# Kernel optimization log

Hardware: AMD Instinct MI355X
Metric: run time of the kernel (lower is better)

The kernel has to match this reference:

```python
import jax, jax.numpy as jnp
import numpy as np

INV_DELTA = 15.0  # init kwarg inv_delta
EPS = 1e-12       # torch F.normalize eps


def setup_inputs() -> dict:
    key = jax.random.key(0)
    k1, k2 = jax.random.split(key)
    features = jax.random.normal(k1, (32, 256, 30, 30), dtype=jnp.float32)
    # _embedding buffer: randn clamped to >= 0
    embedding = jnp.maximum(jax.random.normal(k2, (2048, 256), dtype=jnp.float32), 0.0)
    # _min_distance_mean buffer, initialized to 0.5
    min_distance_mean = jnp.ones((1,), dtype=jnp.float32) * 0.5
    return {"features": features, "embedding": embedding,
            "min_distance_mean": min_distance_mean}


def reference(features, embedding, min_distance_mean):
    # crop 1-pixel border: [B,C,H,W] -> [B,C,H-2,W-2]
    f = features[:, :, 1:-1, 1:-1]
    # squared euclidean distance to each codeword via GEMM trick:
    # dist[b,k,h,w] = ||f[b,:,h,w]||^2 + ||e[k]||^2 - 2 <f, e[k]>
    f2 = jnp.sum(f * f, axis=1, keepdims=True)                 # [B,1,H',W']
    e2 = jnp.sum(embedding * embedding, axis=1)                # [K]
    xe = jnp.einsum('bchw,kc->bkhw', f, embedding)             # 1x1-conv GEMM
    dist = f2 + e2[None, :, None, None] - 2.0 * xe             # [B,K,H',W']
    # adaptive temperature softmax over codewords
    inv_delta_adaptive = INV_DELTA / min_distance_mean[0]
    codes = jax.nn.softmax(-inv_delta_adaptive * dist, axis=1)  # [B,K,H',W']
    # global average pool + L1 normalize
    bow = jnp.mean(codes, axis=(2, 3))                          # [B,K]
    bow = bow / jnp.maximum(jnp.sum(jnp.abs(bow), axis=1, keepdims=True), EPS)
    return (bow, codes)
```

## Files before the change

kernel.cpp:

```cpp
#include <hip/hip_runtime.h>
#include <hip/hip_bf16.h>
#include <math.h>

typedef __attribute__((ext_vector_type(8))) short bf16x8;
typedef __attribute__((ext_vector_type(16))) float f32x16;

#define B_ 32
#define C_ 256
#define K_ 2048
#define HW_ 784
#define NPIX 25088
#define FEAT_BSTRIDE 230400
#define FEAT_CSTRIDE 900
#define INV_DELTA 15.0f
#define LOG2E 1.4426950408889634f
#define QSCALE 409.6f
#define QDEC (LOG2E / QSCALE)

#define BM 128
#define BN 128
#define LSTR 64
#define NSLAB 16

#define AS1 __attribute__((address_space(1)))
#define AS3 __attribute__((address_space(3)))

__device__ __forceinline__ ushort f2bf(float x) {
    __hip_bfloat16 h = __float2bfloat16(x);
    return *reinterpret_cast<ushort*>(&h);
}
__device__ __forceinline__ float bf2f(ushort u) {
    __hip_bfloat16 h;
    *reinterpret_cast<ushort*>(&h) = u;
    return __bfloat162float(h);
}
__device__ __forceinline__ void gl_lds16(const ushort* g, ushort* l) {
    __builtin_amdgcn_global_load_lds((AS1 const uint*)g, (AS3 uint*)l, 16, 0, 0);
}

__global__ void e2_kernel(const float* __restrict__ emb, float* __restrict__ e2) {
    int t = threadIdx.x;
    int wid = t >> 6, lane = t & 63;
    int k = blockIdx.x * 4 + wid;
    const float* er = emb + (size_t)k * C_;
    float v0 = er[lane], v1 = er[lane + 64], v2 = er[lane + 128], v3 = er[lane + 192];
    float s = v0 * v0 + v1 * v1 + v2 * v2 + v3 * v3;
#pragma unroll
    for (int off = 32; off > 0; off >>= 1) s += __shfl_xor(s, off);
    if (lane == 0) e2[k] = s;
}

__global__ void prep_e_kernel(const float* __restrict__ emb,
                              ushort* __restrict__ ehi, ushort* __restrict__ elo) {
    int i = blockIdx.x * 256 + threadIdx.x;
    float v = emb[i];
    ushort h = f2bf(v);
    float r = v - bf2f(h);
    ehi[i] = h;
    elo[i] = f2bf(r);
}

__global__ __launch_bounds__(256) void prep_f_kernel(const float* __restrict__ feat,
                                                     ushort* __restrict__ fhi,
                                                     ushort* __restrict__ flo) {
    __shared__ float F[256 * 65];
    int t = threadIdx.x;
    int px0 = blockIdx.x * 64;
    {
        int lane = t & 63, cq = t >> 6;
        int px = px0 + lane;
        int b = px / HW_, hw = px % HW_;
        int h = hw / 28, w = hw % 28;
        const float* base = feat + (size_t)b * FEAT_BSTRIDE + (size_t)(h + 1) * 30 + (w + 1);
#pragma unroll
        for (int cc = 0; cc < 64; ++cc) {
            int c = cq * 64 + cc;
            F[c * 65 + lane] = base[(size_t)c * FEAT_CSTRIDE];
        }
    }
    __syncthreads();
    {
        int px_l = t >> 2, cseg = t & 3;
        size_t ob = (size_t)(px0 + px_l) * C_ + cseg * 64;
        uint uh[32], ul[32];
#pragma unroll
        for (int j = 0; j < 32; ++j) {
            float v0 = F[(cseg * 64 + 2 * j) * 65 + px_l];
            float v1 = F[(cseg * 64 + 2 * j + 1) * 65 + px_l];
            ushort h0 = f2bf(v0), h1 = f2bf(v1);
            float r0 = v0 - bf2f(h0), r1 = v1 - bf2f(h1);
            uh[j] = (uint)h0 | ((uint)h1 << 16);
            ul[j] = (uint)f2bf(r0) | ((uint)f2bf(r1) << 16);
        }
#pragma unroll
        for (int j = 0; j < 8; ++j) {
            *reinterpret_cast<uint4*>(&fhi[ob + j * 8]) = *reinterpret_cast<uint4*>(&uh[j * 4]);
            *reinterpret_cast<uint4*>(&flo[ob + j * 8]) = *reinterpret_cast<uint4*>(&ul[j * 4]);
        }
    }
}

__global__ __launch_bounds__(256, 2) void gemm_kernel(
    const ushort* __restrict__ fhi, const ushort* __restrict__ flo,
    const ushort* __restrict__ ehi, const ushort* __restrict__ elo,
    const float* __restrict__ mdm, const float* __restrict__ e2g,
    ushort* __restrict__ zq, float* __restrict__ m_part, float* __restrict__ l_part)
{
    __shared__ __align__(16) ushort smem[4][BM * LSTR];
    __shared__ float redA[2][132];
    __shared__ float redM[132];
    ushort* Ah = smem[0];
    ushort* Al = smem[1];
    ushort* Bh = smem[2];
    ushort* Bl = smem[3];
    uint* zT = reinterpret_cast<uint*>(smem[0]);

    int t = threadIdx.x;
    int lane = t & 63, wid = t >> 6;
    int wrow = wid >> 1, wcol = wid & 1;
    int g = lane >> 5, ci = lane & 31;

    int bid = blockIdx.x;
    int swz = (bid & 7) * 392 + (bid >> 3);
    int tile = swz >> 4, slab = swz & 15;
    int px0 = tile * BM;
    int k0 = slab * BN;

    f32x16 acc[2][2];
#pragma unroll
    for (int mi = 0; mi < 2; ++mi)
#pragma unroll
        for (int ni = 0; ni < 2; ++ni)
            acc[mi][ni] = (f32x16)(0.0f);

    for (int step = 0; step < 4; ++step) {
        int c0 = step * 64;
        __syncthreads();
#pragma unroll
        for (int i = 0; i < 4; ++i) {
            int unit = t + i * 256;
            int row = unit >> 3;
            int usw = (unit & 7) ^ (row & 7);
            size_t ga = (size_t)(px0 + row) * C_ + c0 + usw * 8;
            size_t gb = (size_t)(k0 + row) * C_ + c0 + usw * 8;
            gl_lds16(fhi + ga, &Ah[unit * 8]);
            gl_lds16(flo + ga, &Al[unit * 8]);
            gl_lds16(ehi + gb, &Bh[unit * 8]);
            gl_lds16(elo + gb, &Bl[unit * 8]);
        }
        __syncthreads();

        int x7 = ci & 7;
#pragma unroll
        for (int s = 0; s < 4; ++s) {
            int ucol = ((2 * s + g) ^ x7) * 8;
            bf16x8 ah[2], av[2], bh[2], bv[2];
#pragma unroll
            for (int mi = 0; mi < 2; ++mi) {
                int off = (wrow * 64 + mi * 32 + ci) * LSTR + ucol;
                ah[mi] = *reinterpret_cast<const bf16x8*>(&Ah[off]);
                av[mi] = *reinterpret_cast<const bf16x8*>(&Al[off]);
            }
#pragma unroll
            for (int ni = 0; ni < 2; ++ni) {
                int off = (wcol * 64 + ni * 32 + ci) * LSTR + ucol;
                bh[ni] = *reinterpret_cast<const bf16x8*>(&Bh[off]);
                bv[ni] = *reinterpret_cast<const bf16x8*>(&Bl[off]);
            }
#pragma unroll
            for (int mi = 0; mi < 2; ++mi)
#pragma unroll
                for (int ni = 0; ni < 2; ++ni) {
                    acc[mi][ni] = __builtin_amdgcn_mfma_f32_32x32x16_bf16(ah[mi], bh[ni], acc[mi][ni], 0, 0, 0);
                    acc[mi][ni] = __builtin_amdgcn_mfma_f32_32x32x16_bf16(ah[mi], bv[ni], acc[mi][ni], 0, 0, 0);
                    acc[mi][ni] = __builtin_amdgcn_mfma_f32_32x32x16_bf16(av[mi], bh[ni], acc[mi][ni], 0, 0, 0);
                }
        }
    }

    const float alpha = INV_DELTA / mdm[0];
    float e2v[2];
#pragma unroll
    for (int ni = 0; ni < 2; ++ni) e2v[ni] = e2g[k0 + wcol * 64 + ni * 32 + ci];
#pragma unroll
    for (int mi = 0; mi < 2; ++mi)
#pragma unroll
        for (int ni = 0; ni < 2; ++ni)
            acc[mi][ni] = alpha * (2.0f * acc[mi][ni] - e2v[ni]);

    float ms[2][16];
    {
        float mt[2][16];
#pragma unroll
        for (int mi = 0; mi < 2; ++mi)
#pragma unroll
            for (int r = 0; r < 16; ++r)
                mt[mi][r] = fmaxf(acc[mi][0][r], acc[mi][1][r]);
#pragma unroll
        for (int off = 1; off < 32; off <<= 1)
#pragma unroll
            for (int mi = 0; mi < 2; ++mi)
#pragma unroll
                for (int r = 0; r < 16; ++r)
                    mt[mi][r] = fmaxf(mt[mi][r], __shfl_xor(mt[mi][r], off));
        if (ci == 0) {
#pragma unroll
            for (int mi = 0; mi < 2; ++mi)
#pragma unroll
                for (int r = 0; r < 16; ++r)
                    redA[wcol][wrow * 64 + mi * 32 + (r & 3) + 8 * (r >> 2) + 4 * g] = mt[mi][r];
        }
    }
    __syncthreads();
    if (t < 128) redM[t] = fmaxf(redA[0][t], redA[1][t]);
    __syncthreads();
#pragma unroll
    for (int mi = 0; mi < 2; ++mi)
#pragma unroll
        for (int r = 0; r < 16; ++r)
            ms[mi][r] = redM[wrow * 64 + mi * 32 + (r & 3) + 8 * (r >> 2) + 4 * g];

    {
        float lt[2][16];
#pragma unroll
        for (int mi = 0; mi < 2; ++mi)
#pragma unroll
            for (int r = 0; r < 16; ++r)
                lt[mi][r] = exp2f((acc[mi][0][r] - ms[mi][r]) * LOG2E) +
                            exp2f((acc[mi][1][r] - ms[mi][r]) * LOG2E);
#pragma unroll
        for (int off = 1; off < 32; off <<= 1)
#pragma unroll
            for (int mi = 0; mi < 2; ++mi)
#pragma unroll
                for (int r = 0; r < 16; ++r)
                    lt[mi][r] += __shfl_xor(lt[mi][r], off);
        if (ci == 0) {
#pragma unroll
            for (int mi = 0; mi < 2; ++mi)
#pragma unroll
                for (int r = 0; r < 16; ++r)
                    redA[wcol][wrow * 64 + mi * 32 + (r & 3) + 8 * (r >> 2) + 4 * g] = lt[mi][r];
        }
    }
    __syncthreads();
    if (t < 128) {
        m_part[(size_t)slab * NPIX + px0 + t] = redM[t];
        l_part[(size_t)slab * NPIX + px0 + t] = redA[0][t] + redA[1][t];
    }

#pragma unroll
    for (int mi = 0; mi < 2; ++mi)
#pragma unroll
        for (int ni = 0; ni < 2; ++ni) {
            int kl = wcol * 64 + ni * 32 + ci;
#pragma unroll
            for (int r = 0; r < 16; r += 2) {
                int row = wrow * 64 + mi * 32 + (r & 3) + 8 * (r >> 2) + 4 * g;
                float s0 = fmaxf((acc[mi][ni][r]     - ms[mi][r])     * QSCALE, -32760.f);
                float s1 = fmaxf((acc[mi][ni][r + 1] - ms[mi][r + 1]) * QSCALE, -32760.f);
                int q0 = (int)s0, q1 = (int)s1;
                uint u = ((uint)(ushort)(short)q0) | (((uint)(ushort)(short)q1) << 16);
                int pp = row >> 1;
                int seg = pp >> 2;
                zT[kl * 64 + ((seg ^ (kl & 15)) << 2) + (pp & 3)] = u;
            }
        }
    __syncthreads();

    const uint4* zT4 = reinterpret_cast<const uint4*>(zT);
#pragma unroll
    for (int it = 0; it < 8; ++it) {
        int kl = (t >> 4) + it * 16;
        int seg = t & 15;
        uint4 v = zT4[kl * 16 + (seg ^ (kl & 15))];
        int k = k0 + kl;
        int pxx = px0 + seg * 8;
        int bb = pxx / HW_, hh = pxx - bb * HW_;
        *reinterpret_cast<uint4*>(&zq[((size_t)bb * K_ + k) * HW_ + hh]) = v;
    }
}

__global__ void combine_kernel(const float* __restrict__ m_part, const float* __restrict__ l_part,
                               float* __restrict__ m_fin, float* __restrict__ rl_g) {
    int p = blockIdx.x * 256 + threadIdx.x;
    float m = -3.4e38f;
#pragma unroll
    for (int s = 0; s < NSLAB; ++s) m = fmaxf(m, m_part[(size_t)s * NPIX + p]);
    float l = 0.f;
#pragma unroll
    for (int s = 0; s < NSLAB; ++s)
        l += l_part[(size_t)s * NPIX + p] * exp2f((m_part[(size_t)s * NPIX + p] - m) * LOG2E);
    m_fin[p] = m;
    rl_g[p] = 1.0f / l;
}

__global__ __launch_bounds__(256) void finish_kernel(
    const ushort* __restrict__ zq, const float* __restrict__ m_part,
    const float* __restrict__ m_fin, const float* __restrict__ rl_g,
    float* __restrict__ codes, float* __restrict__ bow)
{
    __shared__ float corr[HW_], rls[HW_];
    __shared__ float bsum[64][4];
    int t = threadIdx.x;
    int kc = blockIdx.x, b = blockIdx.y;
    int slab = kc >> 1;
    for (int i = t; i < HW_; i += 256) {
        int p = b * HW_ + i;
        corr[i] = (m_part[(size_t)slab * NPIX + p] - m_fin[p]) * LOG2E;
        rls[i] = rl_g[p];
    }
    __syncthreads();
    int wid = t >> 6, lane = t & 63;
    for (int kl = 0; kl < 64; ++kl) {
        int k = kc * 64 + kl;
        size_t base = ((size_t)b * K_ + k) * HW_;
        float ssum = 0.f;
        if (t < 196) {
            uint2 raw = *reinterpret_cast<const uint2*>(&zq[base + t * 4]);
            int q0 = (int)(short)(raw.x & 0xffffu), q1 = (int)(short)(raw.x >> 16);
            int q2 = (int)(short)(raw.y & 0xffffu), q3 = (int)(short)(raw.y >> 16);
            float4 out;
            out.x = exp2f(fmaf((float)q0, QDEC, corr[t * 4 + 0])) * rls[t * 4 + 0];
            out.y = exp2f(fmaf((float)q1, QDEC, corr[t * 4 + 1])) * rls[t * 4 + 1];
            out.z = exp2f(fmaf((float)q2, QDEC, corr[t * 4 + 2])) * rls[t * 4 + 2];
            out.w = exp2f(fmaf((float)q3, QDEC, corr[t * 4 + 3])) * rls[t * 4 + 3];
            *reinterpret_cast<float4*>(&codes[base + t * 4]) = out;
            ssum = out.x + out.y + out.z + out.w;
        }
#pragma unroll
        for (int off = 32; off > 0; off >>= 1) ssum += __shfl_xor(ssum, off);
        if (lane == 0) bsum[kl][wid] = ssum;
    }
    __syncthreads();
    if (t < 64) {
        float s = bsum[t][0] + bsum[t][1] + bsum[t][2] + bsum[t][3];
        bow[(size_t)b * K_ + kc * 64 + t] = s * (1.0f / 784.0f);
    }
}

__global__ void bownorm_kernel(float* __restrict__ bow) {
    __shared__ float wred[4];
    __shared__ float denom_s;
    int b = blockIdx.x, t = threadIdx.x;
    float* row = bow + (size_t)b * K_;
    float v[8];
    float s = 0.f;
#pragma unroll
    for (int i = 0; i < 8; ++i) {
        v[i] = row[t + i * 256];
        s += fabsf(v[i]);
    }
#pragma unroll
    for (int off = 32; off > 0; off >>= 1) s += __shfl_xor(s, off);
    int wid = t >> 6, lane = t & 63;
    if (lane == 0) wred[wid] = s;
    __syncthreads();
    if (t == 0) denom_s = fmaxf(wred[0] + wred[1] + wred[2] + wred[3], 1e-12f);
    __syncthreads();
    float denom = denom_s;
#pragma unroll
    for (int i = 0; i < 8; ++i) row[t + i * 256] = v[i] / denom;
}

extern "C" void kernel_launch(void* const* d_in, const int* in_sizes, int n_in,
                              void* d_out, int out_size, void* d_ws, size_t ws_size,
                              hipStream_t stream) {
    const float* feat = (const float*)d_in[0];
    const float* emb  = (const float*)d_in[1];
    const float* mdm  = (const float*)d_in[2];
    float* bow   = (float*)d_out;
    float* codes = bow + (size_t)B_ * K_;

    char* ws = (char*)d_ws;
    size_t off = 0;
    auto alloc = [&](size_t bytes) { char* p = ws + off; off = (off + bytes + 255) & ~(size_t)255; return p; };
    ushort* ehi    = (ushort*)alloc((size_t)K_ * C_ * 2);
    ushort* elo    = (ushort*)alloc((size_t)K_ * C_ * 2);
    float*  e2     = (float*)alloc(K_ * 4);
    float*  m_part = (float*)alloc((size_t)NSLAB * NPIX * 4);
    float*  l_part = (float*)alloc((size_t)NSLAB * NPIX * 4);
    float*  m_fin  = (float*)alloc((size_t)NPIX * 4);
    float*  rl_g   = (float*)alloc((size_t)NPIX * 4);
    ushort* zq     = (ushort*)alloc((size_t)NPIX * K_ * 2);

    ushort* fhi = (ushort*)codes;
    ushort* flo = fhi + (size_t)NPIX * C_;

    e2_kernel<<<512, 256, 0, stream>>>(emb, e2);
    prep_e_kernel<<<2048, 256, 0, stream>>>(emb, ehi, elo);
    prep_f_kernel<<<392, 256, 0, stream>>>(feat, fhi, flo);
    gemm_kernel<<<3136, 256, 0, stream>>>(fhi, flo, ehi, elo, mdm, e2, zq, m_part, l_part);
    combine_kernel<<<98, 256, 0, stream>>>(m_part, l_part, m_fin, rl_g);
    finish_kernel<<<dim3(32, 32), 256, 0, stream>>>(zq, m_part, m_fin, rl_g, codes, bow);
    bownorm_kernel<<<32, 256, 0, stream>>>(bow);
}
```

Baseline: 233.6 us.

## Double-buffer GEMM K-chunks in LDS to overlap loads with MFMA

```diff
diff --git a/kernel.cpp b/kernel.cpp
--- a/kernel.cpp
+++ b/kernel.cpp
@@ -19,7 +19,8 @@
 
 #define BM 128
 #define BN 128
-#define LSTR 64
+#define BKC 32
+#define NCH 8
 #define NSLAB 16
 
 #define AS1 __attribute__((address_space(1)))
@@ -106,14 +107,10 @@
     const float* __restrict__ mdm, const float* __restrict__ e2g,
     ushort* __restrict__ zq, float* __restrict__ m_part, float* __restrict__ l_part)
 {
-    __shared__ __align__(16) ushort smem[4][BM * LSTR];
+    __shared__ __align__(16) ushort smem[2][4][BM * BKC];
     __shared__ float redA[2][132];
     __shared__ float redM[132];
-    ushort* Ah = smem[0];
-    ushort* Al = smem[1];
-    ushort* Bh = smem[2];
-    ushort* Bl = smem[3];
-    uint* zT = reinterpret_cast<uint*>(smem[0]);
+    uint* zT = reinterpret_cast<uint*>(smem);
 
     int t = threadIdx.x;
     int lane = t & 63, wid = t >> 6;
@@ -126,6 +123,24 @@
     int px0 = tile * BM;
     int k0 = slab * BN;
 
+    auto stage = [&](int buf, int ch) {
+        int c0 = ch * BKC;
+#pragma unroll
+        for (int i = 0; i < 2; ++i) {
+            int p = t + i * 256;
+            int rp = p >> 3, q = p & 7;
+            int v = q ^ (rp & 7);
+            int row = rp * 2 + (v >> 2);
+            int cu = (v & 3) * 8;
+            size_t ga = (size_t)(px0 + row) * C_ + c0 + cu;
+            size_t gb = (size_t)(k0 + row) * C_ + c0 + cu;
+            gl_lds16(fhi + ga, &smem[buf][0][p * 8]);
+            gl_lds16(flo + ga, &smem[buf][1][p * 8]);
+            gl_lds16(ehi + gb, &smem[buf][2][p * 8]);
+            gl_lds16(elo + gb, &smem[buf][3][p * 8]);
+        }
+    };
+
     f32x16 acc[2][2];
 #pragma unroll
     for (int mi = 0; mi < 2; ++mi)
@@ -133,39 +148,31 @@
         for (int ni = 0; ni < 2; ++ni)
             acc[mi][ni] = (f32x16)(0.0f);
 
-    for (int step = 0; step < 4; ++step) {
-        int c0 = step * 64;
-        __syncthreads();
-#pragma unroll
-        for (int i = 0; i < 4; ++i) {
-            int unit = t + i * 256;
-            int row = unit >> 3;
-            int usw = (unit & 7) ^ (row & 7);
-            size_t ga = (size_t)(px0 + row) * C_ + c0 + usw * 8;
-            size_t gb = (size_t)(k0 + row) * C_ + c0 + usw * 8;
-            gl_lds16(fhi + ga, &Ah[unit * 8]);
-            gl_lds16(flo + ga, &Al[unit * 8]);
-            gl_lds16(ehi + gb, &Bh[unit * 8]);
-            gl_lds16(elo + gb, &Bl[unit * 8]);
-        }
-        __syncthreads();
-
-        int x7 = ci & 7;
-#pragma unroll
-        for (int s = 0; s < 4; ++s) {
-            int ucol = ((2 * s + g) ^ x7) * 8;
+    int xr = (ci >> 1) & 7;
+    int bb4 = (ci & 1) * 4;
+    int rpA0 = wrow * 32 + (ci >> 1);
+    int rpB0 = wcol * 32 + (ci >> 1);
+
+    stage(0, 0);
+    __syncthreads();
+    for (int ch = 0; ch < NCH; ++ch) {
+        if (ch + 1 < NCH) stage((ch + 1) & 1, ch + 1);
+        int cur = ch & 1;
+#pragma unroll
+        for (int s = 0; s < 2; ++s) {
+            int qs = (bb4 + s * 2 + g) ^ xr;
             bf16x8 ah[2], av[2], bh[2], bv[2];
 #pragma unroll
             for (int mi = 0; mi < 2; ++mi) {
-                int off = (wrow * 64 + mi * 32 + ci) * LSTR + ucol;
-                ah[mi] = *reinterpret_cast<const bf16x8*>(&Ah[off]);
-                av[mi] = *reinterpret_cast<const bf16x8*>(&Al[off]);
+                int off = (rpA0 + mi * 16) * 64 + qs * 8;
+                ah[mi] = *reinterpret_cast<const bf16x8*>(&smem[cur][0][off]);
+                av[mi] = *reinterpret_cast<const bf16x8*>(&smem[cur][1][off]);
             }
 #pragma unroll
             for (int ni = 0; ni < 2; ++ni) {
-                int off = (wcol * 64 + ni * 32 + ci) * LSTR + ucol;
-                bh[ni] = *reinterpret_cast<const bf16x8*>(&Bh[off]);
-                bv[ni] = *reinterpret_cast<const bf16x8*>(&Bl[off]);
+                int off = (rpB0 + ni * 16) * 64 + qs * 8;
+                bh[ni] = *reinterpret_cast<const bf16x8*>(&smem[cur][2][off]);
+                bv[ni] = *reinterpret_cast<const bf16x8*>(&smem[cur][3][off]);
             }
 #pragma unroll
             for (int mi = 0; mi < 2; ++mi)
@@ -176,6 +183,7 @@
                     acc[mi][ni] = __builtin_amdgcn_mfma_f32_32x32x16_bf16(av[mi], bh[ni], acc[mi][ni], 0, 0, 0);
                 }
         }
+        __syncthreads();
     }
 
     const float alpha = INV_DELTA / mdm[0];
```

New measurement: 236.5 us. About the same (+1.2%).

## Load MFMA operands directly from global memory, dropping LDS staging

Applied to the files above, without the earlier changes.

```diff
diff --git a/kernel.cpp b/kernel.cpp
--- a/kernel.cpp
+++ b/kernel.cpp
@@ -19,11 +19,7 @@
 
 #define BM 128
 #define BN 128
-#define LSTR 64
 #define NSLAB 16
-
-#define AS1 __attribute__((address_space(1)))
-#define AS3 __attribute__((address_space(3)))
 
 __device__ __forceinline__ ushort f2bf(float x) {
     __hip_bfloat16 h = __float2bfloat16(x);
@@ -33,9 +29,6 @@
     __hip_bfloat16 h;
     *reinterpret_cast<ushort*>(&h) = u;
     return __bfloat162float(h);
-}
-__device__ __forceinline__ void gl_lds16(const ushort* g, ushort* l) {
-    __builtin_amdgcn_global_load_lds((AS1 const uint*)g, (AS3 uint*)l, 16, 0, 0);
 }
 
 __global__ void e2_kernel(const float* __restrict__ emb, float* __restrict__ e2) {
@@ -100,20 +93,15 @@
     }
 }
 
-__global__ __launch_bounds__(256, 2) void gemm_kernel(
+__global__ __launch_bounds__(256, 3) void gemm_kernel(
     const ushort* __restrict__ fhi, const ushort* __restrict__ flo,
     const ushort* __restrict__ ehi, const ushort* __restrict__ elo,
     const float* __restrict__ mdm, const float* __restrict__ e2g,
     ushort* __restrict__ zq, float* __restrict__ m_part, float* __restrict__ l_part)
 {
-    __shared__ __align__(16) ushort smem[4][BM * LSTR];
     __shared__ float redA[2][132];
     __shared__ float redM[132];
-    ushort* Ah = smem[0];
-    ushort* Al = smem[1];
-    ushort* Bh = smem[2];
-    ushort* Bl = smem[3];
-    uint* zT = reinterpret_cast<uint*>(smem[0]);
+    __shared__ uint zT[8192];
 
     int t = threadIdx.x;
     int lane = t & 63, wid = t >> 6;
@@ -126,6 +114,23 @@
     int px0 = tile * BM;
     int k0 = slab * BN;
 
+    const ushort* pah[2];
+    const ushort* pal[2];
+    const ushort* pbh[2];
+    const ushort* pbl[2];
+#pragma unroll
+    for (int mi = 0; mi < 2; ++mi) {
+        size_t r = (size_t)(px0 + wrow * 64 + mi * 32 + ci) * C_ + g * 8;
+        pah[mi] = fhi + r;
+        pal[mi] = flo + r;
+    }
+#pragma unroll
+    for (int ni = 0; ni < 2; ++ni) {
+        size_t r = (size_t)(k0 + wcol * 64 + ni * 32 + ci) * C_ + g * 8;
+        pbh[ni] = ehi + r;
+        pbl[ni] = elo + r;
+    }
+
     f32x16 acc[2][2];
 #pragma unroll
     for (int mi = 0; mi < 2; ++mi)
@@ -133,39 +138,21 @@
         for (int ni = 0; ni < 2; ++ni)
             acc[mi][ni] = (f32x16)(0.0f);
 
-    for (int step = 0; step < 4; ++step) {
-        int c0 = step * 64;
-        __syncthreads();
-#pragma unroll
-        for (int i = 0; i < 4; ++i) {
-            int unit = t + i * 256;
-            int row = unit >> 3;
-            int usw = (unit & 7) ^ (row & 7);
-            size_t ga = (size_t)(px0 + row) * C_ + c0 + usw * 8;
-            size_t gb = (size_t)(k0 + row) * C_ + c0 + usw * 8;
-            gl_lds16(fhi + ga, &Ah[unit * 8]);
-            gl_lds16(flo + ga, &Al[unit * 8]);
-            gl_lds16(ehi + gb, &Bh[unit * 8]);
-            gl_lds16(elo + gb, &Bl[unit * 8]);
-        }
-        __syncthreads();
-
-        int x7 = ci & 7;
-#pragma unroll
-        for (int s = 0; s < 4; ++s) {
-            int ucol = ((2 * s + g) ^ x7) * 8;
+#pragma unroll 2
+    for (int ch = 0; ch < 8; ++ch) {
+#pragma unroll
+        for (int s = 0; s < 2; ++s) {
+            int off = ch * 32 + s * 16;
             bf16x8 ah[2], av[2], bh[2], bv[2];
 #pragma unroll
             for (int mi = 0; mi < 2; ++mi) {
-                int off = (wrow * 64 + mi * 32 + ci) * LSTR + ucol;
-                ah[mi] = *reinterpret_cast<const bf16x8*>(&Ah[off]);
-                av[mi] = *reinterpret_cast<const bf16x8*>(&Al[off]);
+                ah[mi] = *reinterpret_cast<const bf16x8*>(pah[mi] + off);
+                av[mi] = *reinterpret_cast<const bf16x8*>(pal[mi] + off);
             }
 #pragma unroll
             for (int ni = 0; ni < 2; ++ni) {
-                int off = (wcol * 64 + ni * 32 + ci) * LSTR + ucol;
-                bh[ni] = *reinterpret_cast<const bf16x8*>(&Bh[off]);
-                bv[ni] = *reinterpret_cast<const bf16x8*>(&Bl[off]);
+                bh[ni] = *reinterpret_cast<const bf16x8*>(pbh[ni] + off);
+                bv[ni] = *reinterpret_cast<const bf16x8*>(pbl[ni] + off);
             }
 #pragma unroll
             for (int mi = 0; mi < 2; ++mi)
```

After: 294.3 us. 26.0% more time.
